# Optimization experiments

Hardware: AMD Instinct MI355X
Metric: run time of the kernel (lower is better)

The kernel has to match this reference:

```python
import jax, jax.numpy as jnp
import numpy as np

B, S, E, H, F = 8, 1024, 1024, 16, 4096
D = E // H  # head_dim = 64
EPS = 1e-5


def setup_inputs() -> dict:
    key = jax.random.key(0)
    ks = jax.random.split(key, 12)
    s = 0.02
    return {
        "x": jax.random.normal(ks[0], (B, S, E), dtype=jnp.float32),
        # per-head projections (shared across heads), torch stores [out,in]; we use [in,out]
        "Wq": jax.random.normal(ks[1], (D, D), dtype=jnp.float32) * s,
        "Wk": jax.random.normal(ks[2], (D, D), dtype=jnp.float32) * s,
        "Wv": jax.random.normal(ks[3], (D, D), dtype=jnp.float32) * s,
        "Wo": jax.random.normal(ks[4], (E, E), dtype=jnp.float32) * s,
        "bo": jnp.zeros((E,), dtype=jnp.float32),
        "W1": jax.random.normal(ks[5], (E, F), dtype=jnp.float32) * s,
        "b1": jnp.zeros((F,), dtype=jnp.float32),
        "W2": jax.random.normal(ks[6], (F, E), dtype=jnp.float32) * s,
        "b2": jnp.zeros((E,), dtype=jnp.float32),
        "g1": jnp.ones((E,), dtype=jnp.float32),
        "beta1": jnp.zeros((E,), dtype=jnp.float32),
        "g2": jnp.ones((E,), dtype=jnp.float32),
        "beta2": jnp.zeros((E,), dtype=jnp.float32),
    }


def _layer_norm(x, g, b):
    m = jnp.mean(x, axis=-1, keepdims=True)
    v = jnp.mean(jnp.square(x - m), axis=-1, keepdims=True)
    return (x - m) * jax.lax.rsqrt(v + EPS) * g + b


def reference(x, Wq, Wk, Wv, Wo, bo, W1, b1, W2, b2, g1, beta1, g2, beta2):
    b, s, e = x.shape
    # --- attention sublayer (pre-norm) ---
    nx = _layer_norm(x, g1, beta1)
    h = nx.reshape(b, s, H, D)              # [B,S,H,D]
    q = h @ Wq                               # per-head linear, weight shared over heads
    k = h @ Wk
    v = h @ Wv
    energy = jnp.einsum('bqhd,bkhd->bhqk', q, k)  # full [B,H,S,S] scores
    mask = jnp.tril(jnp.ones((s, s), dtype=bool))
    energy = jnp.where(mask, energy, -jnp.inf)
    att = jax.nn.softmax(energy / jnp.sqrt(jnp.float32(e)), axis=-1)  # NOTE: scale by sqrt(embed_dim)
    o = jnp.einsum('bhqk,bkhd->bqhd', att, v).reshape(b, s, e)
    x = x + (o @ Wo + bo)
    # --- MLP sublayer (pre-norm); dropout is identity in eval ---
    nx = _layer_norm(x, g2, beta2)
    x = x + (jax.nn.relu(nx @ W1 + b1) @ W2 + b2)
    return x
```

## Files before the change

kernel.cpp:

```cpp
#include <hip/hip_runtime.h>

typedef unsigned short u16;
typedef __attribute__((ext_vector_type(4))) float f4;
typedef __attribute__((ext_vector_type(8))) short s8v;
typedef __attribute__((ext_vector_type(4))) unsigned short u16x4;

#define DEVINL __device__ __forceinline__

DEVINL float b2f(u16 u) { union { unsigned i; float f; } x; x.i = ((unsigned)u) << 16; return x.f; }
DEVINL u16 f2b(float f) {
  union { float f; unsigned i; } x; x.f = f;
  unsigned r = 0x7FFFu + ((x.i >> 16) & 1u);
  return (u16)((x.i + r) >> 16);
}

#define GLD_LDS16(g, l)                                                        \
  __builtin_amdgcn_global_load_lds((__attribute__((address_space(1))) void*)(g), \
                                   (__attribute__((address_space(3))) void*)(l), 16, 0, 0)

__global__ __launch_bounds__(256) void k_transpose_all(
    const float* __restrict__ Wo, const float* __restrict__ W1,
    const float* __restrict__ W2, const float* __restrict__ Wq,
    const float* __restrict__ Wk, const float* __restrict__ Wv,
    u16* __restrict__ WoT, u16* __restrict__ W1T, u16* __restrict__ W2T,
    u16* __restrict__ WqT, u16* __restrict__ WkT, u16* __restrict__ WvT) {
  int id = blockIdx.x;
  const float* in;
  u16* out;
  int R, C, bx, by;
  if (id < 1024) {
    in = Wo; out = WoT; R = 1024; C = 1024; bx = id & 31; by = id >> 5;
  } else if (id < 5120) {
    int t = id - 1024;
    in = W1; out = W1T; R = 1024; C = 4096; bx = t & 127; by = t >> 7;
  } else if (id < 9216) {
    int t = id - 5120;
    in = W2; out = W2T; R = 4096; C = 1024; bx = t & 31; by = t >> 5;
  } else {
    int t = id - 9216;
    int z = t >> 2;
    in = z == 0 ? Wq : (z == 1 ? Wk : Wv);
    out = z == 0 ? WqT : (z == 1 ? WkT : WvT);
    R = 64; C = 64; bx = t & 1; by = (t >> 1) & 1;
  }
  __shared__ float tt[32][33];
  int tx = threadIdx.x & 31, ty = threadIdx.x >> 5;
  int c0 = bx * 32, r0 = by * 32;
#pragma unroll
  for (int i = 0; i < 32; i += 8)
    tt[ty + i][tx] = in[(long)(r0 + ty + i) * C + (c0 + tx)];
  __syncthreads();
#pragma unroll
  for (int i = 0; i < 32; i += 8)
    out[(long)(c0 + ty + i) * R + (r0 + tx)] = f2b(tt[tx][ty + i]);
}

__global__ __launch_bounds__(256) void k_vtrans(const u16* __restrict__ v, u16* __restrict__ vt) {
  __shared__ u16 t[64][72];
  int bh = blockIdx.x, b = bh >> 4, h = bh & 15;
  int s0 = blockIdx.y * 64;
  int tid = threadIdx.x;
#pragma unroll
  for (int p = 0; p < 2; ++p) {
    int idx = p * 256 + tid;
    int sl = idx >> 3, c8 = (idx & 7) * 8;
    *(s8v*)(&t[sl][c8]) = *(const s8v*)(v + (((long)(b * 1024 + s0 + sl) * 16 + h) * 64) + c8);
  }
  __syncthreads();
#pragma unroll
  for (int p = 0; p < 2; ++p) {
    int idx = p * 256 + tid;
    int d = idx >> 3, c8 = (idx & 7) * 8;
    s8v o;
#pragma unroll
    for (int e = 0; e < 8; ++e) o[e] = (short)t[c8 + e][d];
    *(s8v*)(vt + ((long)bh * 64 + d) * 1024 + s0 + c8) = o;
  }
}

__global__ __launch_bounds__(256) void k_layernorm(const float* __restrict__ x,
                                                   const float* __restrict__ g,
                                                   const float* __restrict__ be,
                                                   u16* __restrict__ out) {
  long row = blockIdx.x;
  int tid = threadIdx.x;
  f4 v = ((const f4*)(x + row * 1024))[tid];
  float s = v[0] + v[1] + v[2] + v[3];
  float s2 = v[0] * v[0] + v[1] * v[1] + v[2] * v[2] + v[3] * v[3];
#pragma unroll
  for (int off = 32; off > 0; off >>= 1) {
    s += __shfl_down(s, off, 64);
    s2 += __shfl_down(s2, off, 64);
  }
  __shared__ float red[8];
  int wv = tid >> 6, ln = tid & 63;
  if (ln == 0) { red[wv] = s; red[4 + wv] = s2; }
  __syncthreads();
  s = red[0] + red[1] + red[2] + red[3];
  s2 = red[4] + red[5] + red[6] + red[7];
  float mean = s * (1.0f / 1024.0f);
  float var = s2 * (1.0f / 1024.0f) - mean * mean;
  float rs = rsqrtf(var + 1e-5f);
  f4 gg = ((const f4*)g)[tid];
  f4 bb = ((const f4*)be)[tid];
  u16x4 o;
#pragma unroll
  for (int i = 0; i < 4; ++i) o[i] = f2b((v[i] - mean) * rs * gg[i] + bb[i]);
  ((u16x4*)(out + row * 1024))[tid] = o;
}

__global__ __launch_bounds__(256) void k_ln_qkv(
    const float* __restrict__ x, const float* __restrict__ g, const float* __restrict__ be,
    const u16* __restrict__ WqT, const u16* __restrict__ WkT, const u16* __restrict__ WvT,
    u16* __restrict__ q, u16* __restrict__ k, u16* __restrict__ v) {
  constexpr int LDP = 72;
  __shared__ u16 A[64 * LDP];
  int tid = threadIdx.x, lane = tid & 63, wave = tid >> 6;
  int quad = lane >> 4, l16 = lane & 15;
  long xrow = (long)blockIdx.x * 4 + wave;
  const f4* xp = (const f4*)(x + xrow * 1024);
  const f4* gp = (const f4*)g;
  const f4* bp = (const f4*)be;
  f4 vv[4];
  float s = 0.f, s2 = 0.f;
#pragma unroll
  for (int j = 0; j < 4; ++j) {
    vv[j] = xp[lane * 4 + j];
#pragma unroll
    for (int e = 0; e < 4; ++e) { s += vv[j][e]; s2 += vv[j][e] * vv[j][e]; }
  }
#pragma unroll
  for (int off = 1; off < 64; off <<= 1) {
    s += __shfl_xor(s, off, 64);
    s2 += __shfl_xor(s2, off, 64);
  }
  float mean = s * (1.0f / 1024.0f);
  float var = s2 * (1.0f / 1024.0f) - mean * mean;
  float rs = rsqrtf(var + 1e-5f);
  u16* ap = &A[(wave * 16 + (lane >> 2)) * LDP + (lane & 3) * 16];
#pragma unroll
  for (int j = 0; j < 4; ++j) {
    f4 gg = gp[lane * 4 + j], bb = bp[lane * 4 + j];
    u16x4 o;
#pragma unroll
    for (int e = 0; e < 4; ++e) o[e] = f2b((vv[j][e] - mean) * rs * gg[e] + bb[e]);
    *(u16x4*)(ap + j * 4) = o;
  }
  __syncthreads();
  s8v a0 = *(const s8v*)(&A[(wave * 16 + l16) * LDP + quad * 8]);
  s8v a1 = *(const s8v*)(&A[(wave * 16 + l16) * LDP + 32 + quad * 8]);
  long rbase = (long)blockIdx.x * 64 + wave * 16;
  const u16* Ws[3] = {WqT, WkT, WvT};
  u16* Os[3] = {q, k, v};
#pragma unroll
  for (int t = 0; t < 3; ++t) {
#pragma unroll
    for (int j = 0; j < 4; ++j) {
      s8v b0 = *(const s8v*)(Ws[t] + (j * 16 + l16) * 64 + quad * 8);
      s8v b1 = *(const s8v*)(Ws[t] + (j * 16 + l16) * 64 + 32 + quad * 8);
      f4 acc = {0.f, 0.f, 0.f, 0.f};
      acc = __builtin_amdgcn_mfma_f32_16x16x32_bf16(a0, b0, acc, 0, 0, 0);
      acc = __builtin_amdgcn_mfma_f32_16x16x32_bf16(a1, b1, acc, 0, 0, 0);
#pragma unroll
      for (int r = 0; r < 4; ++r)
        Os[t][(rbase + quad * 4 + r) * 64 + j * 16 + l16] = f2b(acc[r]);
    }
  }
}

__global__ __launch_bounds__(256) void k_attn_mfma(const u16* __restrict__ q,
                                                   const u16* __restrict__ kk,
                                                   const u16* __restrict__ vt,
                                                   u16* __restrict__ o) {
  constexpr int LDK = 72;
  __shared__ u16 Ks[2][64 * LDK];
  __shared__ u16 Vt[2][64 * LDK];
  __shared__ u16 Ps[4][16 * LDK];
  int tid = threadIdx.x, lane = tid & 63, wave = tid >> 6;
  int quad = lane >> 4, l16 = lane & 15;
  int b = blockIdx.x >> 4, h = blockIdx.x & 15;
  int qi = (int)gridDim.y - 1 - (int)blockIdx.y;
  int q0 = qi * 64 + wave * 16;

  const u16* qp = q + (((long)(b * 1024 + q0 + l16)) * 16 + h) * 64;
  s8v aq0 = *(const s8v*)(qp + quad * 8);
  s8v aq1 = *(const s8v*)(qp + 32 + quad * 8);

  int srow0 = tid >> 3, sc8 = (tid & 7) * 8;
  int srow1 = srow0 + 32;
  const u16* kb_ = kk + (long)b * 1048576 + h * 64;
  const u16* vb_ = vt + (long)blockIdx.x * 65536;

  f4 O[4];
  float m_[4], l_[4];
#pragma unroll
  for (int jd = 0; jd < 4; ++jd) O[jd] = f4{0.f, 0.f, 0.f, 0.f};
#pragma unroll
  for (int r = 0; r < 4; ++r) { m_[r] = -__builtin_inff(); l_[r] = 0.f; }

  s8v rk0 = *(const s8v*)(kb_ + (long)srow0 * 1024 + sc8);
  s8v rk1 = *(const s8v*)(kb_ + (long)srow1 * 1024 + sc8);
  s8v rv0 = *(const s8v*)(vb_ + (long)srow0 * 1024 + sc8);
  s8v rv1 = *(const s8v*)(vb_ + (long)srow1 * 1024 + sc8);
  *(s8v*)(&Ks[0][srow0 * LDK + sc8]) = rk0;
  *(s8v*)(&Ks[0][srow1 * LDK + sc8]) = rk1;
  *(s8v*)(&Vt[0][srow0 * LDK + sc8]) = rv0;
  *(s8v*)(&Vt[0][srow1 * LDK + sc8]) = rv1;

  for (int kt = 0; kt <= qi; ++kt) {
    int cur = kt & 1;
    if (kt < qi) {
      long ko = (long)(kt + 1) * 64;
      rk0 = *(const s8v*)(kb_ + (ko + srow0) * 1024 + sc8);
      rk1 = *(const s8v*)(kb_ + (ko + srow1) * 1024 + sc8);
      rv0 = *(const s8v*)(vb_ + (long)srow0 * 1024 + (kt + 1) * 64 + sc8);
      rv1 = *(const s8v*)(vb_ + (long)srow1 * 1024 + (kt + 1) * 64 + sc8);
    }
    __syncthreads();

    const u16* Kc = Ks[cur];
    const u16* Vc = Vt[cur];
    f4 sf[4];
    __builtin_amdgcn_s_setprio(1);
#pragma unroll
    for (int jn = 0; jn < 4; ++jn) {
      s8v b0 = *(const s8v*)(Kc + (jn * 16 + l16) * LDK + quad * 8);
      s8v b1 = *(const s8v*)(Kc + (jn * 16 + l16) * LDK + 32 + quad * 8);
      f4 acc = f4{0.f, 0.f, 0.f, 0.f};
      acc = __builtin_amdgcn_mfma_f32_16x16x32_bf16(aq0, b0, acc, 0, 0, 0);
      acc = __builtin_amdgcn_mfma_f32_16x16x32_bf16(aq1, b1, acc, 0, 0, 0);
      sf[jn] = acc;
    }
    __builtin_amdgcn_s_setprio(0);
    bool diag = (kt == qi);
    float rm[4];
#pragma unroll
    for (int r = 0; r < 4; ++r) rm[r] = -__builtin_inff();
#pragma unroll
    for (int jn = 0; jn < 4; ++jn)
#pragma unroll
      for (int r = 0; r < 4; ++r) {
        float v = sf[jn][r] * 0.03125f;
        if (diag && (jn * 16 + l16 > wave * 16 + quad * 4 + r)) v = -__builtin_inff();
        sf[jn][r] = v;
        rm[r] = fmaxf(rm[r], v);
      }
#pragma unroll
    for (int off = 1; off < 16; off <<= 1)
#pragma unroll
      for (int r = 0; r < 4; ++r) rm[r] = fmaxf(rm[r], __shfl_xor(rm[r], off, 64));
    bool ok = (rm[0] <= m_[0] + 8.f) && (rm[1] <= m_[1] + 8.f) &&
              (rm[2] <= m_[2] + 8.f) && (rm[3] <= m_[3] + 8.f);
    if (!__all(ok)) {
#pragma unroll
      for (int r = 0; r < 4; ++r) {
        float mn = fmaxf(m_[r], rm[r]);
        float alpha = __expf(m_[r] - mn);
        m_[r] = mn;
        l_[r] *= alpha;
#pragma unroll
        for (int jd = 0; jd < 4; ++jd) O[jd][r] *= alpha;
      }
    }
    float rs[4];
#pragma unroll
    for (int r = 0; r < 4; ++r) rs[r] = 0.f;
#pragma unroll
    for (int jn = 0; jn < 4; ++jn)
#pragma unroll
      for (int r = 0; r < 4; ++r) {
        float p = __expf(sf[jn][r] - m_[r]);
        rs[r] += p;
        Ps[wave][(quad * 4 + r) * LDK + jn * 16 + l16] = f2b(p);
      }
#pragma unroll
    for (int off = 1; off < 16; off <<= 1)
#pragma unroll
      for (int r = 0; r < 4; ++r) rs[r] += __shfl_xor(rs[r], off, 64);
#pragma unroll
    for (int r = 0; r < 4; ++r) l_[r] += rs[r];
    asm volatile("s_waitcnt lgkmcnt(0)" ::: "memory");
    s8v p0 = *(const s8v*)(&Ps[wave][l16 * LDK + quad * 8]);
    s8v p1 = *(const s8v*)(&Ps[wave][l16 * LDK + 32 + quad * 8]);
    __builtin_amdgcn_s_setprio(1);
#pragma unroll
    for (int jd = 0; jd < 4; ++jd) {
      s8v b0 = *(const s8v*)(Vc + (jd * 16 + l16) * LDK + quad * 8);
      s8v b1 = *(const s8v*)(Vc + (jd * 16 + l16) * LDK + 32 + quad * 8);
      O[jd] = __builtin_amdgcn_mfma_f32_16x16x32_bf16(p0, b0, O[jd], 0, 0, 0);
      O[jd] = __builtin_amdgcn_mfma_f32_16x16x32_bf16(p1, b1, O[jd], 0, 0, 0);
    }
    __builtin_amdgcn_s_setprio(0);

    if (kt < qi) {
      int nb = cur ^ 1;
      *(s8v*)(&Ks[nb][srow0 * LDK + sc8]) = rk0;
      *(s8v*)(&Ks[nb][srow1 * LDK + sc8]) = rk1;
      *(s8v*)(&Vt[nb][srow0 * LDK + sc8]) = rv0;
      *(s8v*)(&Vt[nb][srow1 * LDK + sc8]) = rv1;
    }
  }
#pragma unroll
  for (int r = 0; r < 4; ++r) {
    float inv = 1.0f / l_[r];
    u16* op = o + (((long)(b * 1024 + q0 + quad * 4 + r)) * 16 + h) * 64;
#pragma unroll
    for (int jd = 0; jd < 4; ++jd) op[jd * 16 + l16] = f2b(O[jd][r] * inv);
  }
}

template <int EPI>
__global__ __launch_bounds__(512) void k_gemm256(const u16* __restrict__ A,
                                                 const u16* __restrict__ BT,
                                                 const float* __restrict__ bias,
                                                 const float* __restrict__ resid,
                                                 void* __restrict__ outp, int M, int N, int K,
                                                 int lda) {
  __shared__ __align__(16) u16 S[65536];
  int tid = threadIdx.x, lane = tid & 63, wave = tid >> 6;
  int l16 = lane & 15, quad = lane >> 4;
  int wm = wave >> 2, wn = wave & 3;
  long bm = blockIdx.x, bn = blockIdx.y;
  int z = blockIdx.z;

  int rl = l16 & 7;
  int c0 = 8 * (quad ^ rl);
  int c1 = 8 * ((quad ^ 4) ^ rl);
  int rowA = (wm * 64 + l16) * 64;
  int rowB = (wn * 32 + l16) * 64;

  int Lb = tid * 16;
  int Ls = Lb ^ (((Lb >> 7) & 7) << 4);
  int r_ = Ls >> 7, kin = (Ls & 127) >> 1;
  const u16* pA = A + (bm * 256 + r_) * (long)lda + kin + (long)z * K;
  const u16* pB = BT + (bn * 256 + r_) * (long)lda + kin + (long)z * K;

  f4 acc[4][4][2];
#pragma unroll
  for (int q = 0; q < 4; ++q)
#pragma unroll
    for (int mi = 0; mi < 4; ++mi)
#pragma unroll
      for (int nj = 0; nj < 2; ++nj) acc[q][mi][nj] = f4{0.f, 0.f, 0.f, 0.f};
  s8v aF[4][2], bF[2][2][2];

#define BAR asm volatile("s_barrier" ::: "memory")
#define LGK0 asm volatile("s_waitcnt lgkmcnt(0)" ::: "memory")
#define WVM4 asm volatile("s_waitcnt vmcnt(4)" ::: "memory")
#define WVM0 asm volatile("s_waitcnt vmcnt(0)" ::: "memory")

#define STAGE(mat, half, t, buf)                                               \
  do {                                                                         \
    const u16* g_ = ((mat) ? pB : pA) + (long)(half) * 128 * lda + (t) * 64;   \
    char* l_ = ((char*)S) + ((buf) * 32768 + (mat) * 16384 + (half) * 8192) * 2 + wave * 1024; \
    GLD_LDS16(g_, l_);                                                         \
    GLD_LDS16(g_ + 64 * (long)lda, l_ + 8192);                                 \
  } while (0)

#define LDA(buf, mh)                                                           \
  do {                                                                         \
    const u16* p_ = S + (buf) * 32768 + (mh) * 8192 + rowA;                    \
    _Pragma("unroll") for (int mi = 0; mi < 4; ++mi) {                         \
      aF[mi][0] = *(const s8v*)(p_ + mi * 1024 + c0);                          \
      aF[mi][1] = *(const s8v*)(p_ + mi * 1024 + c1);                          \
    }                                                                          \
  } while (0)

#define LDB(buf, nh, set)                                                      \
  do {                                                                         \
    const u16* p_ = S + (buf) * 32768 + 16384 + (nh) * 8192 + rowB;            \
    _Pragma("unroll") for (int nj = 0; nj < 2; ++nj) {                         \
      bF[set][nj][0] = *(const s8v*)(p_ + nj * 1024 + c0);                     \
      bF[set][nj][1] = *(const s8v*)(p_ + nj * 1024 + c1);                     \
    }                                                                          \
  } while (0)

#define MM(q)                                                                  \
  do {                                                                         \
    _Pragma("unroll") for (int mi = 0; mi < 4; ++mi)                           \
        _Pragma("unroll") for (int nj = 0; nj < 2; ++nj) {                     \
      acc[q][mi][nj] = __builtin_amdgcn_mfma_f32_16x16x32_bf16(                \
          aF[mi][0], bF[(q) & 1][nj][0], acc[q][mi][nj], 0, 0, 0);             \
      acc[q][mi][nj] = __builtin_amdgcn_mfma_f32_16x16x32_bf16(                \
          aF[mi][1], bF[(q) & 1][nj][1], acc[q][mi][nj], 0, 0, 0);             \
    }                                                                          \
  } while (0)

#define PHASES(t, LAST)                                                        \
  LDA(0, 0); LDB(0, 0, 0); STAGE(0, 1, (t) + 1, 1);                            \
  BAR; LGK0; __builtin_amdgcn_s_setprio(1); MM(0); __builtin_amdgcn_s_setprio(0); BAR; \
  LDB(0, 1, 1); STAGE(1, 1, (t) + 1, 1);                                       \
  BAR; LGK0; __builtin_amdgcn_s_setprio(1); MM(1); __builtin_amdgcn_s_setprio(0); BAR; \
  LDA(0, 1); if (!(LAST)) STAGE(0, 0, (t) + 2, 0);                             \
  BAR; LGK0; __builtin_amdgcn_s_setprio(1); MM(2); __builtin_amdgcn_s_setprio(0); BAR; \
  if (!(LAST)) STAGE(1, 0, (t) + 2, 0);                                        \
  __builtin_amdgcn_s_setprio(1); MM(3); __builtin_amdgcn_s_setprio(0);         \
  if (LAST) { WVM0; } else { WVM4; }                                           \
  BAR;                                                                         \
  LDA(1, 0); LDB(1, 0, 0); if (!(LAST)) STAGE(0, 1, (t) + 2, 0);               \
  BAR; LGK0; __builtin_amdgcn_s_setprio(1); MM(0); __builtin_amdgcn_s_setprio(0); BAR; \
  LDB(1, 1, 1); if (!(LAST)) STAGE(1, 1, (t) + 2, 0);                          \
  BAR; LGK0; __builtin_amdgcn_s_setprio(1); MM(1); __builtin_amdgcn_s_setprio(0); BAR; \
  LDA(1, 1); if (!(LAST)) STAGE(0, 0, (t) + 3, 1);                             \
  BAR; LGK0; __builtin_amdgcn_s_setprio(1); MM(2); __builtin_amdgcn_s_setprio(0); BAR; \
  if (!(LAST)) STAGE(1, 0, (t) + 3, 1);                                        \
  __builtin_amdgcn_s_setprio(1); MM(3); __builtin_amdgcn_s_setprio(0);         \
  if (!(LAST)) { WVM4; BAR; }

  STAGE(0, 0, 0, 0);
  STAGE(1, 0, 0, 0);
  STAGE(0, 1, 0, 0);
  STAGE(1, 1, 0, 0);
  STAGE(0, 0, 1, 1);
  STAGE(1, 0, 1, 1);
  WVM4; BAR;

  int NI = K >> 7;
  for (int i = 0; i < NI - 1; ++i) {
    int t = 2 * i;
    PHASES(t, 0);
  }
  {
    int t = 2 * (NI - 1);
    PHASES(t, 1);
  }

#undef PHASES
#undef MM
#undef LDB
#undef LDA
#undef STAGE
#undef WVM0
#undef WVM4
#undef LGK0
#undef BAR

  if (EPI == 1) {
    __syncthreads();
    int trow = tid >> 4, tcol = (tid & 15) * 8;
#pragma unroll
    for (int q = 0; q < 4; ++q) {
      int mh = q >> 1, nh = q & 1;
#pragma unroll
      for (int nj = 0; nj < 2; ++nj) {
        int c_loc = wn * 32 + nj * 16 + l16;
        float bcol = bias[(int)bn * 256 + nh * 128 + c_loc];
#pragma unroll
        for (int mi = 0; mi < 4; ++mi)
#pragma unroll
          for (int rr = 0; rr < 4; ++rr) {
            int r_loc = wm * 64 + mi * 16 + quad * 4 + rr;
            float val = acc[q][mi][nj][rr] + bcol;
            S[r_loc * 132 + c_loc] = f2b(val > 0.f ? val : 0.f);
          }
      }
      __syncthreads();
#pragma unroll
      for (int p = 0; p < 4; ++p) {
        int r_loc = p * 32 + trow;
        s8v v8 = *(const s8v*)(S + r_loc * 132 + tcol);
        long grow = bm * 256 + mh * 128 + r_loc;
        *(s8v*)((u16*)outp + grow * (long)N + (int)bn * 256 + nh * 128 + tcol) = v8;
      }
      __syncthreads();
    }
  } else {
    float* P0 = (EPI == 0) ? ((float*)outp + (long)z * M * N) : nullptr;
#pragma unroll
    for (int q = 0; q < 4; ++q) {
      int mh = q >> 1, nh = q & 1;
#pragma unroll
      for (int mi = 0; mi < 4; ++mi) {
#pragma unroll
        for (int nj = 0; nj < 2; ++nj) {
          long row = bm * 256 + mh * 128 + wm * 64 + mi * 16 + quad * 4;
          int col = (int)bn * 256 + nh * 128 + wn * 32 + nj * 16 + l16;
#pragma unroll
          for (int rr = 0; rr < 4; ++rr) {
            float val = acc[q][mi][nj][rr];
            if (EPI == 0) {
              P0[(row + rr) * (long)N + col] = val;
            } else {
              ((float*)outp)[(row + rr) * (long)N + col] =
                  resid[(row + rr) * (long)N + col] + val + bias[col];
            }
          }
        }
      }
    }
  }
}

__global__ __launch_bounds__(512) void k_gemm256n128(const u16* __restrict__ A,
                                                     const u16* __restrict__ BT,
                                                     const float* __restrict__ bias,
                                                     const float* __restrict__ resid,
                                                     float* __restrict__ outp,
                                                     int M, int N, int K, int lda) {
  __shared__ __align__(16) u16 S[49152];
  int tid = threadIdx.x, lane = tid & 63, wave = tid >> 6;
  int l16 = lane & 15, quad = lane >> 4;
  int wm = wave >> 1, wn = wave & 1;
  long bm = blockIdx.x, bn = blockIdx.y;

  int rl = l16 & 7;
  int c0 = 8 * (quad ^ rl);
  int c1 = 8 * ((quad ^ 4) ^ rl);
  int rowA = (wm >> 1) * 8192 + ((wm & 1) * 64 + l16) * 64;
  int rowB = 16384 + (wn * 64 + l16) * 64;

  int Lb = tid * 16;
  int Ls = Lb ^ (((Lb >> 7) & 7) << 4);
  int r_ = Ls >> 7, kin = (Ls & 127) >> 1;
  const u16* pA = A + (bm * 256 + r_) * (long)lda + kin;
  const u16* pB = BT + (bn * 128 + r_) * (long)lda + kin;

  f4 acc[4][4];
#pragma unroll
  for (int mi = 0; mi < 4; ++mi)
#pragma unroll
    for (int nj = 0; nj < 4; ++nj) acc[mi][nj] = f4{0.f, 0.f, 0.f, 0.f};
  s8v aF[4][2], bF[2][2];

#define BAR asm volatile("s_barrier" ::: "memory")
#define LGK0 asm volatile("s_waitcnt lgkmcnt(0)" ::: "memory")
#define WVM4 asm volatile("s_waitcnt vmcnt(4)" ::: "memory")
#define WVM0 asm volatile("s_waitcnt vmcnt(0)" ::: "memory")

#define STAGEA(t, buf)                                                         \
  do {                                                                         \
    const u16* g_ = pA + (t) * 64;                                             \
    char* l_ = ((char*)S) + (buf) * 49152 + wave * 1024;                       \
    GLD_LDS16(g_, l_);                                                         \
    GLD_LDS16(g_ + 64 * (long)lda, l_ + 8192);                                 \
    GLD_LDS16(g_ + 128 * (long)lda, l_ + 16384);                               \
    GLD_LDS16(g_ + 192 * (long)lda, l_ + 24576);                               \
  } while (0)

#define STAGEB(t, buf)                                                         \
  do {                                                                         \
    const u16* g_ = pB + (t) * 64;                                             \
    char* l_ = ((char*)S) + (buf) * 49152 + 32768 + wave * 1024;               \
    GLD_LDS16(g_, l_);                                                         \
    GLD_LDS16(g_ + 64 * (long)lda, l_ + 8192);                                 \
  } while (0)

#define LDAn(buf)                                                              \
  do {                                                                         \
    const u16* p_ = S + (buf) * 24576 + rowA;                                  \
    _Pragma("unroll") for (int mi = 0; mi < 4; ++mi) {                         \
      aF[mi][0] = *(const s8v*)(p_ + mi * 1024 + c0);                          \
      aF[mi][1] = *(const s8v*)(p_ + mi * 1024 + c1);                          \
    }                                                                          \
  } while (0)

#define LDBn(buf, nh)                                                          \
  do {                                                                         \
    const u16* p_ = S + (buf) * 24576 + rowB + (nh) * 2048;                    \
    _Pragma("unroll") for (int nj2 = 0; nj2 < 2; ++nj2) {                      \
      bF[nj2][0] = *(const s8v*)(p_ + nj2 * 1024 + c0);                        \
      bF[nj2][1] = *(const s8v*)(p_ + nj2 * 1024 + c1);                        \
    }                                                                          \
  } while (0)

#define MMn(nh)                                                                \
  do {                                                                         \
    _Pragma("unroll") for (int mi = 0; mi < 4; ++mi)                           \
        _Pragma("unroll") for (int nj2 = 0; nj2 < 2; ++nj2) {                  \
      acc[mi][(nh) * 2 + nj2] = __builtin_amdgcn_mfma_f32_16x16x32_bf16(       \
          aF[mi][0], bF[nj2][0], acc[mi][(nh) * 2 + nj2], 0, 0, 0);            \
      acc[mi][(nh) * 2 + nj2] = __builtin_amdgcn_mfma_f32_16x16x32_bf16(       \
          aF[mi][1], bF[nj2][1], acc[mi][(nh) * 2 + nj2], 0, 0, 0);            \
    }                                                                          \
  } while (0)

#define PHASES(t, LAST)                                                        \
  LDAn(0); LDBn(0, 0); STAGEB((t) + 1, 1);                                     \
  BAR; LGK0; __builtin_amdgcn_s_setprio(1); MMn(0); __builtin_amdgcn_s_setprio(0); BAR; \
  LDBn(0, 1); if (!(LAST)) STAGEA((t) + 2, 0);                                 \
  BAR; LGK0; __builtin_amdgcn_s_setprio(1); MMn(1); __builtin_amdgcn_s_setprio(0); \
  if (LAST) { WVM0; } else { WVM4; }                                           \
  BAR;                                                                         \
  LDAn(1); LDBn(1, 0); if (!(LAST)) STAGEB((t) + 2, 0);                        \
  BAR; LGK0; __builtin_amdgcn_s_setprio(1); MMn(0); __builtin_amdgcn_s_setprio(0); BAR; \
  LDBn(1, 1); if (!(LAST)) STAGEA((t) + 3, 1);                                 \
  BAR; LGK0; __builtin_amdgcn_s_setprio(1); MMn(1); __builtin_amdgcn_s_setprio(0); \
  if (!(LAST)) { WVM4; }                                                       \
  BAR;

  STAGEA(0, 0);
  STAGEB(0, 0);
  STAGEA(1, 1);
  WVM4; BAR;

  int NI = K >> 7;
  for (int i = 0; i < NI - 1; ++i) {
    int t = 2 * i;
    PHASES(t, 0);
  }
  {
    int t = 2 * (NI - 1);
    PHASES(t, 1);
  }

#undef PHASES
#undef MMn
#undef LDBn
#undef LDAn
#undef STAGEB
#undef STAGEA
#undef WVM0
#undef WVM4
#undef LGK0
#undef BAR

#pragma unroll
  for (int mi = 0; mi < 4; ++mi) {
#pragma unroll
    for (int nj = 0; nj < 4; ++nj) {
      long row = bm * 256 + wm * 64 + mi * 16 + quad * 4;
      int col = (int)bn * 128 + wn * 64 + nj * 16 + l16;
      float bcol = bias[col];
#pragma unroll
      for (int rr = 0; rr < 4; ++rr) {
        outp[(row + rr) * (long)N + col] =
            resid[(row + rr) * (long)N + col] + acc[mi][nj][rr] + bcol;
      }
    }
  }
}

extern "C" void kernel_launch(void* const* d_in, const int* in_sizes, int n_in, void* d_out,
                              int out_size, void* d_ws, size_t ws_size, hipStream_t stream) {
  const float* x = (const float*)d_in[0];
  const float* Wq = (const float*)d_in[1];
  const float* Wk = (const float*)d_in[2];
  const float* Wv = (const float*)d_in[3];
  const float* Wo = (const float*)d_in[4];
  const float* bo = (const float*)d_in[5];
  const float* W1 = (const float*)d_in[6];
  const float* b1 = (const float*)d_in[7];
  const float* W2 = (const float*)d_in[8];
  const float* b2 = (const float*)d_in[9];
  const float* g1 = (const float*)d_in[10];
  const float* be1 = (const float*)d_in[11];
  const float* g2 = (const float*)d_in[12];
  const float* be2 = (const float*)d_in[13];

  char* ws = (char*)d_ws;
  const size_t MB = 1ull << 20;
  u16* nx = (u16*)(ws + 0);
  u16* qb = (u16*)(ws + 16 * MB);
  u16* kb = (u16*)(ws + 32 * MB);
  u16* vb = (u16*)(ws + 48 * MB);
  float* x1 = (float*)(ws + 64 * MB);
  u16* h1 = (u16*)(ws + 96 * MB);
  u16* vtr = (u16*)(ws + 96 * MB);
  u16* WoT = (u16*)(ws + 160 * MB);
  u16* W1T = (u16*)(ws + 162 * MB);
  u16* W2T = (u16*)(ws + 170 * MB);
  u16* WqT = (u16*)(ws + 178 * MB);
  u16* WkT = WqT + 64 * 64;
  u16* WvT = WkT + 64 * 64;
  u16* ob = nx;
  u16* nx2 = qb;

  k_transpose_all<<<9228, 256, 0, stream>>>(Wo, W1, W2, Wq, Wk, Wv, WoT, W1T, W2T, WqT, WkT, WvT);

  k_ln_qkv<<<2048, 256, 0, stream>>>(x, g1, be1, WqT, WkT, WvT, qb, kb, vb);
  k_vtrans<<<dim3(128, 16), 256, 0, stream>>>(vb, vtr);
  k_attn_mfma<<<dim3(128, 16), 256, 0, stream>>>(qb, kb, vtr, ob);
  k_gemm256n128<<<dim3(32, 8), 512, 0, stream>>>(ob, WoT, bo, x, x1, 8192, 1024, 1024, 1024);

  k_layernorm<<<8192, 256, 0, stream>>>(x1, g2, be2, nx2);
  k_gemm256<1><<<dim3(32, 16, 1), 512, 0, stream>>>(nx2, W1T, b1, nullptr, h1, 8192, 4096, 1024, 1024);
  k_gemm256n128<<<dim3(32, 8), 512, 0, stream>>>(h1, W2T, b2, x1, (float*)d_out, 8192, 1024, 4096, 4096);
}
```

Measured before the change: 402.2 us.

## Enlarge attention query tile to 128 rows with 8 waves sharing K/V tiles

The causal flash-attention kernel now uses 512 threads (8 waves) covering 128 query rows per block instead of 64, halving the grid in the query dimension. Each 64-row K/V tile loaded into LDS is reused by twice as many query rows, which halves global K/V traffic and the per-thread staging loads. The second half of the waves processes one extra diagonal key tile, while the first half idles on that last iteration but still hits the barriers, so some work imbalance and fewer blocks for load balancing are the trade-off.

```diff
diff --git a/kernel.cpp b/kernel.cpp
--- a/kernel.cpp
+++ b/kernel.cpp
@@ -168,26 +168,27 @@
   }
 }
 
-__global__ __launch_bounds__(256) void k_attn_mfma(const u16* __restrict__ q,
+__global__ __launch_bounds__(512) void k_attn_mfma(const u16* __restrict__ q,
                                                    const u16* __restrict__ kk,
                                                    const u16* __restrict__ vt,
                                                    u16* __restrict__ o) {
   constexpr int LDK = 72;
   __shared__ u16 Ks[2][64 * LDK];
   __shared__ u16 Vt[2][64 * LDK];
-  __shared__ u16 Ps[4][16 * LDK];
+  __shared__ u16 Ps[8][16 * LDK];
   int tid = threadIdx.x, lane = tid & 63, wave = tid >> 6;
   int quad = lane >> 4, l16 = lane & 15;
   int b = blockIdx.x >> 4, h = blockIdx.x & 15;
   int qi = (int)gridDim.y - 1 - (int)blockIdx.y;
-  int q0 = qi * 64 + wave * 16;
+  int q0 = qi * 128 + wave * 16;
+  int myNt = 2 * qi + (wave >> 2);
+  int lastKt = 2 * qi + 1;
 
   const u16* qp = q + (((long)(b * 1024 + q0 + l16)) * 16 + h) * 64;
   s8v aq0 = *(const s8v*)(qp + quad * 8);
   s8v aq1 = *(const s8v*)(qp + 32 + quad * 8);
 
-  int srow0 = tid >> 3, sc8 = (tid & 7) * 8;
-  int srow1 = srow0 + 32;
+  int srow = tid >> 3, sc8 = (tid & 7) * 8;
   const u16* kb_ = kk + (long)b * 1048576 + h * 64;
   const u16* vb_ = vt + (long)blockIdx.x * 65536;
 
@@ -198,106 +199,101 @@
 #pragma unroll
   for (int r = 0; r < 4; ++r) { m_[r] = -__builtin_inff(); l_[r] = 0.f; }
 
-  s8v rk0 = *(const s8v*)(kb_ + (long)srow0 * 1024 + sc8);
-  s8v rk1 = *(const s8v*)(kb_ + (long)srow1 * 1024 + sc8);
-  s8v rv0 = *(const s8v*)(vb_ + (long)srow0 * 1024 + sc8);
-  s8v rv1 = *(const s8v*)(vb_ + (long)srow1 * 1024 + sc8);
-  *(s8v*)(&Ks[0][srow0 * LDK + sc8]) = rk0;
-  *(s8v*)(&Ks[0][srow1 * LDK + sc8]) = rk1;
-  *(s8v*)(&Vt[0][srow0 * LDK + sc8]) = rv0;
-  *(s8v*)(&Vt[0][srow1 * LDK + sc8]) = rv1;
-
-  for (int kt = 0; kt <= qi; ++kt) {
+  s8v rk0 = *(const s8v*)(kb_ + (long)srow * 1024 + sc8);
+  s8v rv0 = *(const s8v*)(vb_ + (long)srow * 1024 + sc8);
+  *(s8v*)(&Ks[0][srow * LDK + sc8]) = rk0;
+  *(s8v*)(&Vt[0][srow * LDK + sc8]) = rv0;
+
+  for (int kt = 0; kt <= lastKt; ++kt) {
     int cur = kt & 1;
-    if (kt < qi) {
+    if (kt < lastKt) {
       long ko = (long)(kt + 1) * 64;
-      rk0 = *(const s8v*)(kb_ + (ko + srow0) * 1024 + sc8);
-      rk1 = *(const s8v*)(kb_ + (ko + srow1) * 1024 + sc8);
-      rv0 = *(const s8v*)(vb_ + (long)srow0 * 1024 + (kt + 1) * 64 + sc8);
-      rv1 = *(const s8v*)(vb_ + (long)srow1 * 1024 + (kt + 1) * 64 + sc8);
+      rk0 = *(const s8v*)(kb_ + (ko + srow) * 1024 + sc8);
+      rv0 = *(const s8v*)(vb_ + (long)srow * 1024 + (kt + 1) * 64 + sc8);
     }
     __syncthreads();
 
-    const u16* Kc = Ks[cur];
-    const u16* Vc = Vt[cur];
-    f4 sf[4];
-    __builtin_amdgcn_s_setprio(1);
-#pragma unroll
-    for (int jn = 0; jn < 4; ++jn) {
-      s8v b0 = *(const s8v*)(Kc + (jn * 16 + l16) * LDK + quad * 8);
-      s8v b1 = *(const s8v*)(Kc + (jn * 16 + l16) * LDK + 32 + quad * 8);
-      f4 acc = f4{0.f, 0.f, 0.f, 0.f};
-      acc = __builtin_amdgcn_mfma_f32_16x16x32_bf16(aq0, b0, acc, 0, 0, 0);
-      acc = __builtin_amdgcn_mfma_f32_16x16x32_bf16(aq1, b1, acc, 0, 0, 0);
-      sf[jn] = acc;
+    if (kt <= myNt) {
+      const u16* Kc = Ks[cur];
+      const u16* Vc = Vt[cur];
+      f4 sf[4];
+      __builtin_amdgcn_s_setprio(1);
+#pragma unroll
+      for (int jn = 0; jn < 4; ++jn) {
+        s8v b0 = *(const s8v*)(Kc + (jn * 16 + l16) * LDK + quad * 8);
+        s8v b1 = *(const s8v*)(Kc + (jn * 16 + l16) * LDK + 32 + quad * 8);
+        f4 acc = f4{0.f, 0.f, 0.f, 0.f};
+        acc = __builtin_amdgcn_mfma_f32_16x16x32_bf16(aq0, b0, acc, 0, 0, 0);
+        acc = __builtin_amdgcn_mfma_f32_16x16x32_bf16(aq1, b1, acc, 0, 0, 0);
+        sf[jn] = acc;
+      }
+      __builtin_amdgcn_s_setprio(0);
+      bool diag = (kt == myNt);
+      int rloc = (wave & 3) * 16 + quad * 4;
+      float rm[4];
+#pragma unroll
+      for (int r = 0; r < 4; ++r) rm[r] = -__builtin_inff();
+#pragma unroll
+      for (int jn = 0; jn < 4; ++jn)
+#pragma unroll
+        for (int r = 0; r < 4; ++r) {
+          float v = sf[jn][r] * 0.03125f;
+          if (diag && (jn * 16 + l16 > rloc + r)) v = -__builtin_inff();
+          sf[jn][r] = v;
+          rm[r] = fmaxf(rm[r], v);
+        }
+#pragma unroll
+      for (int off = 1; off < 16; off <<= 1)
+#pragma unroll
+        for (int r = 0; r < 4; ++r) rm[r] = fmaxf(rm[r], __shfl_xor(rm[r], off, 64));
+      bool ok = (rm[0] <= m_[0] + 8.f) && (rm[1] <= m_[1] + 8.f) &&
+                (rm[2] <= m_[2] + 8.f) && (rm[3] <= m_[3] + 8.f);
+      if (!__all(ok)) {
+#pragma unroll
+        for (int r = 0; r < 4; ++r) {
+          float mn = fmaxf(m_[r], rm[r]);
+          float alpha = __expf(m_[r] - mn);
+          m_[r] = mn;
+          l_[r] *= alpha;
+#pragma unroll
+          for (int jd = 0; jd < 4; ++jd) O[jd][r] *= alpha;
+        }
+      }
+      float rs[4];
+#pragma unroll
+      for (int r = 0; r < 4; ++r) rs[r] = 0.f;
+#pragma unroll
+      for (int jn = 0; jn < 4; ++jn)
+#pragma unroll
+        for (int r = 0; r < 4; ++r) {
+          float p = __expf(sf[jn][r] - m_[r]);
+          rs[r] += p;
+          Ps[wave][(quad * 4 + r) * LDK + jn * 16 + l16] = f2b(p);
+        }
+#pragma unroll
+      for (int off = 1; off < 16; off <<= 1)
+#pragma unroll
+        for (int r = 0; r < 4; ++r) rs[r] += __shfl_xor(rs[r], off, 64);
+#pragma unroll
+      for (int r = 0; r < 4; ++r) l_[r] += rs[r];
+      asm volatile("s_waitcnt lgkmcnt(0)" ::: "memory");
+      s8v p0 = *(const s8v*)(&Ps[wave][l16 * LDK + quad * 8]);
+      s8v p1 = *(const s8v*)(&Ps[wave][l16 * LDK + 32 + quad * 8]);
+      __builtin_amdgcn_s_setprio(1);
+#pragma unroll
+      for (int jd = 0; jd < 4; ++jd) {
+        s8v b0 = *(const s8v*)(Vc + (jd * 16 + l16) * LDK + quad * 8);
+        s8v b1 = *(const s8v*)(Vc + (jd * 16 + l16) * LDK + 32 + quad * 8);
+        O[jd] = __builtin_amdgcn_mfma_f32_16x16x32_bf16(p0, b0, O[jd], 0, 0, 0);
+        O[jd] = __builtin_amdgcn_mfma_f32_16x16x32_bf16(p1, b1, O[jd], 0, 0, 0);
+      }
+      __builtin_amdgcn_s_setprio(0);
     }
-    __builtin_amdgcn_s_setprio(0);
-    bool diag = (kt == qi);
-    float rm[4];
-#pragma unroll
-    for (int r = 0; r < 4; ++r) rm[r] = -__builtin_inff();
-#pragma unroll
-    for (int jn = 0; jn < 4; ++jn)
-#pragma unroll
-      for (int r = 0; r < 4; ++r) {
-        float v = sf[jn][r] * 0.03125f;
-        if (diag && (jn * 16 + l16 > wave * 16 + quad * 4 + r)) v = -__builtin_inff();
-        sf[jn][r] = v;
-        rm[r] = fmaxf(rm[r], v);
-      }
-#pragma unroll
-    for (int off = 1; off < 16; off <<= 1)
-#pragma unroll
-      for (int r = 0; r < 4; ++r) rm[r] = fmaxf(rm[r], __shfl_xor(rm[r], off, 64));
-    bool ok = (rm[0] <= m_[0] + 8.f) && (rm[1] <= m_[1] + 8.f) &&
-              (rm[2] <= m_[2] + 8.f) && (rm[3] <= m_[3] + 8.f);
-    if (!__all(ok)) {
-#pragma unroll
-      for (int r = 0; r < 4; ++r) {
-        float mn = fmaxf(m_[r], rm[r]);
-        float alpha = __expf(m_[r] - mn);
-        m_[r] = mn;
-        l_[r] *= alpha;
-#pragma unroll
-        for (int jd = 0; jd < 4; ++jd) O[jd][r] *= alpha;
-      }
-    }
-    float rs[4];
-#pragma unroll
-    for (int r = 0; r < 4; ++r) rs[r] = 0.f;
-#pragma unroll
-    for (int jn = 0; jn < 4; ++jn)
-#pragma unroll
-      for (int r = 0; r < 4; ++r) {
-        float p = __expf(sf[jn][r] - m_[r]);
-        rs[r] += p;
-        Ps[wave][(quad * 4 + r) * LDK + jn * 16 + l16] = f2b(p);
-      }
-#pragma unroll
-    for (int off = 1; off < 16; off <<= 1)
-#pragma unroll
-      for (int r = 0; r < 4; ++r) rs[r] += __shfl_xor(rs[r], off, 64);
-#pragma unroll
-    for (int r = 0; r < 4; ++r) l_[r] += rs[r];
-    asm volatile("s_waitcnt lgkmcnt(0)" ::: "memory");
-    s8v p0 = *(const s8v*)(&Ps[wave][l16 * LDK + quad * 8]);
-    s8v p1 = *(const s8v*)(&Ps[wave][l16 * LDK + 32 + quad * 8]);
-    __builtin_amdgcn_s_setprio(1);
-#pragma unroll
-    for (int jd = 0; jd < 4; ++jd) {
-      s8v b0 = *(const s8v*)(Vc + (jd * 16 + l16) * LDK + quad * 8);
-      s8v b1 = *(const s8v*)(Vc + (jd * 16 + l16) * LDK + 32 + quad * 8);
-      O[jd] = __builtin_amdgcn_mfma_f32_16x16x32_bf16(p0, b0, O[jd], 0, 0, 0);
-      O[jd] = __builtin_amdgcn_mfma_f32_16x16x32_bf16(p1, b1, O[jd], 0, 0, 0);
-    }
-    __builtin_amdgcn_s_setprio(0);
-
-    if (kt < qi) {
-      int nb = cur ^ 1;
-      *(s8v*)(&Ks[nb][srow0 * LDK + sc8]) = rk0;
-      *(s8v*)(&Ks[nb][srow1 * LDK + sc8]) = rk1;
-      *(s8v*)(&Vt[nb][srow0 * LDK + sc8]) = rv0;
-      *(s8v*)(&Vt[nb][srow1 * LDK + sc8]) = rv1;
+
+    if (kt < lastKt) {
+      int nb = (cur ^ 1);
+      *(s8v*)(&Ks[nb][srow * LDK + sc8]) = rk0;
+      *(s8v*)(&Vt[nb][srow * LDK + sc8]) = rv0;
     }
   }
 #pragma unroll
@@ -669,7 +665,7 @@
 
   k_ln_qkv<<<2048, 256, 0, stream>>>(x, g1, be1, WqT, WkT, WvT, qb, kb, vb);
   k_vtrans<<<dim3(128, 16), 256, 0, stream>>>(vb, vtr);
-  k_attn_mfma<<<dim3(128, 16), 256, 0, stream>>>(qb, kb, vtr, ob);
+  k_attn_mfma<<<dim3(128, 8), 512, 0, stream>>>(qb, kb, vtr, ob);
   k_gemm256n128<<<dim3(32, 8), 512, 0, stream>>>(ob, WoT, bo, x, x1, 8192, 1024, 1024, 1024);
 
   k_layernorm<<<8192, 256, 0, stream>>>(x1, g2, be2, nx2);
```

Measured after the change: 400.8 us. About the same (-0.4%).
